# Performance work log

Measured on AMD Instinct MI355X. Metric: run time of the kernel, lower is better.

The kernel has to match this reference:

```python
import jax, jax.numpy as jnp
import numpy as np

EPS = 1e-08

def _householder(x, v):
    # x: [B,S,r], v: [B,S,r]; H x = x - 2 v_n (v_n . x), v_n = v/||v||
    v_norm_sq = jnp.sum(v * v, axis=-1, keepdims=True) + EPS
    v_n = v / jnp.sqrt(v_norm_sq)
    vTx = jnp.sum(x * v_n, axis=-1, keepdims=True)
    return x - 2.0 * v_n * vTx

def setup_inputs() -> dict:
    key = jax.random.key(0)
    ks = jax.random.split(key, 8)
    B, S, D, R = 4, 4096, 1024, 256
    N_IN, N_PROC, N_OUT, K = 16, 64, 16, 8
    x = jax.random.normal(ks[0], (B, S, D), dtype=jnp.float32)
    input_idx = jax.random.randint(ks[1], (B, S), 0, N_IN)
    process_indices = jax.random.randint(ks[2], (B, S, K), 0, N_PROC)
    output_idx = jax.random.randint(ks[3], (B, S), 0, N_OUT)
    # learned params (orthogonal-ish init approximated by scaled gaussian)
    input_neurons = jax.random.normal(ks[4], (N_IN, D, R), dtype=jnp.float32) / np.sqrt(D)
    pv = jax.random.normal(ks[5], (N_PROC, R), dtype=jnp.float32)
    process_neurons = pv / (jnp.linalg.norm(pv, axis=-1, keepdims=True) + EPS)
    output_neurons = jax.random.normal(ks[6], (N_OUT, R, D), dtype=jnp.float32) / np.sqrt(D)
    return {"x": x, "input_neurons": input_neurons, "process_neurons": process_neurons,
            "output_neurons": output_neurons, "input_idx": input_idx,
            "process_indices": process_indices, "output_idx": output_idx}

def reference(x, input_neurons, process_neurons, output_neurons,
              input_idx, process_indices, output_idx):
    # ---- input projection (hard selection): d_model -> rank ----
    # compute all-expert projections then gather per token (avoids [B,S,D,R] gather)
    all_in = jnp.einsum('bsd,ndr->bsnr', x, input_neurons)          # [B,S,n_in,R]
    h = jnp.take_along_axis(all_in, input_idx[..., None, None], axis=2)[:, :, 0, :]  # [B,S,R]
    # ---- process: k sequential Householder reflections ----
    selected_v = process_neurons[process_indices]                    # [B,S,k,R]
    vs = jnp.moveaxis(selected_v, 2, 0)                              # [k,B,S,R]
    def step(carry, v):
        return _householder(carry, v), None
    h, _ = jax.lax.scan(step, h, vs)
    # ---- output projection (hard selection): rank -> d_model ----
    all_out = jnp.einsum('bsr,nrd->bsnd', h, output_neurons)         # [B,S,n_out,D]
    out = jnp.take_along_axis(all_out, output_idx[..., None, None], axis=2)[:, :, 0, :]
    return out
```

## Files before the change

### kernel.cpp

```cpp
#include <hip/hip_runtime.h>
#include <hip/hip_bf16.h>

#define NT    16384
#define DM    1024
#define RK    256
#define N_IN  16
#define N_OUT 16
#define KHH   8
#define MAXTOK 1536
#define BM    64
#define TPE   (MAXTOK / BM)
#define KC    4

typedef short bf16x8 __attribute__((ext_vector_type(8)));
typedef float f32x4 __attribute__((ext_vector_type(4)));
typedef unsigned short u16;
typedef u16 u16x8 __attribute__((ext_vector_type(8)));
typedef u16 u16x4 __attribute__((ext_vector_type(4)));

__device__ __forceinline__ u16 f2bf(float f) {
  __hip_bfloat16 b = __float2bfloat16(f);
  return *reinterpret_cast<u16*>(&b);
}
__device__ __forceinline__ float bf2f(u16 u) {
  return __uint_as_float((unsigned)u << 16);
}

__device__ __forceinline__ void gl_lds16(const void* g, void* lds) {
  __builtin_amdgcn_global_load_lds(
      (const __attribute__((address_space(1))) void*)g,
      (__attribute__((address_space(3))) void*)lds, 16, 0, 0);
}

__global__ __launch_bounds__(256) void build_lists_pn(
    const int* __restrict__ in_idx, const int* __restrict__ out_idx,
    const float* __restrict__ pn,
    int* __restrict__ list_in, int* __restrict__ cnt_in,
    int* __restrict__ list_out, int* __restrict__ cnt_out,
    float* __restrict__ pnorm2) {
  const int b = blockIdx.x;
  const int tid = threadIdx.x, lane = tid & 63, wid = tid >> 6;

  if (b == 32) {
    const int p = tid >> 2, q = tid & 3;
    const float* row = pn + (size_t)p * RK + q * 64;
    float s = 0.f;
#pragma unroll
    for (int i = 0; i < 16; i++) {
      const float4 v = ((const float4*)row)[i];
      s += v.x * v.x + v.y * v.y + v.z * v.z + v.w * v.w;
    }
    s += __shfl_xor(s, 1);
    s += __shfl_xor(s, 2);
    if (q == 0) pnorm2[p] = s + 1e-8f;
    return;
  }

  const int e = b & 15, which = b >> 4;
  const int* __restrict__ idx = which ? out_idx : in_idx;
  int* __restrict__ list = (which ? list_out : list_in) + (size_t)e * NT;
  int* __restrict__ cnt = (which ? cnt_out : cnt_in) + e;

  __shared__ int wsum[4];
  const unsigned long long lt = (1ull << lane) - 1ull;
  int off = 0;
  for (int base = 0; base < NT; base += 1024) {
    const int4 iv = ((const int4*)(idx + base))[tid];
    const bool f0 = iv.x == e, f1 = iv.y == e, f2 = iv.z == e, f3 = iv.w == e;
    const unsigned long long m0 = __ballot(f0), m1 = __ballot(f1),
                             m2 = __ballot(f2), m3 = __ballot(f3);
    const int below = __popcll(m0 & lt) + __popcll(m1 & lt) +
                      __popcll(m2 & lt) + __popcll(m3 & lt);
    const int wtot = __popcll(m0) + __popcll(m1) + __popcll(m2) + __popcll(m3);
    if (lane == 0) wsum[wid] = wtot;
    __syncthreads();
    int b0 = 0, tot = 0;
#pragma unroll
    for (int w = 0; w < 4; w++) { if (w < wid) b0 += wsum[w]; tot += wsum[w]; }
    int pos = off + b0 + below;
    const int t = base + tid * 4;
    if (f0) list[pos++] = t;
    if (f1) list[pos++] = t + 1;
    if (f2) list[pos++] = t + 2;
    if (f3) list[pos++] = t + 3;
    off += tot;
    __syncthreads();
  }
  if (tid == 0) *cnt = off;
}

__global__ __launch_bounds__(256) void transpose_cvt2(
    const float* __restrict__ Win, const float* __restrict__ Wout,
    u16* __restrict__ WinT, u16* __restrict__ WoT) {
  const int z = blockIdx.z;
  const float* __restrict__ src = z ? Wout : Win;
  u16* __restrict__ dst = z ? WoT : WinT;
  const int R = z ? RK : DM, C = z ? DM : RK;
  const int e = blockIdx.y;
  const int tilesC = C >> 6;
  const int tr = (blockIdx.x / tilesC) << 6;
  const int tc = (blockIdx.x % tilesC) << 6;
  __shared__ float ls[64][65];
  const int t = threadIdx.x;
  const int row = t >> 2, q = t & 3;
  const float* s = src + (size_t)e * R * C + (size_t)(tr + row) * C + tc + q * 16;
#pragma unroll
  for (int j = 0; j < 4; j++) {
    const float4 v = ((const float4*)s)[j];
    ls[row][q * 16 + j * 4 + 0] = v.x;
    ls[row][q * 16 + j * 4 + 1] = v.y;
    ls[row][q * 16 + j * 4 + 2] = v.z;
    ls[row][q * 16 + j * 4 + 3] = v.w;
  }
  __syncthreads();
  const int cc = t >> 2;
  u16x8 o0, o1;
#pragma unroll
  for (int j = 0; j < 8; j++) o0[j] = f2bf(ls[q * 16 + j][cc]);
#pragma unroll
  for (int j = 0; j < 8; j++) o1[j] = f2bf(ls[q * 16 + 8 + j][cc]);
  u16* d = dst + (size_t)e * C * R + (size_t)(tc + cc) * R + tr + q * 16;
  ((u16x8*)d)[0] = o0;
  ((u16x8*)d)[1] = o1;
}

__global__ __launch_bounds__(256, 6) void input_gemm_part(
    const float* __restrict__ x, const u16* __restrict__ WinT,
    const int* __restrict__ list, const int* __restrict__ cnt,
    u16* __restrict__ h4) {
  const int bid = blockIdx.x;
  const int xcd = bid & 7;
  int j = bid >> 3;
  const int tile = j % TPE;
  j /= TPE;
  const int nb = j & 1;
  const int e = xcd * 2 + ((j >> 1) & 1);
  const int kc = j >> 2;
  const int nt = cnt[e];
  const int t0 = tile * BM;
  if (t0 >= nt) return;
  const int* __restrict__ lst = list + (size_t)e * NT + t0;
  const int ntok = min(BM, nt - t0);

  __shared__ __align__(16) u16 As[BM * 64];
  __shared__ __align__(16) u16 Bs[128 * 64];
  __shared__ int toks[BM];

  const int tid = threadIdx.x, lane = tid & 63, w = tid >> 6;
  if (tid < BM) toks[tid] = lst[tid < ntok ? tid : 0];
  __syncthreads();

  const int arow = tid >> 3, k8 = tid & 7;
  const float* axp0 = x + (size_t)toks[arow] * DM + kc * 256 + k8 * 8;
  const float* axp1 = x + (size_t)toks[arow + 32] * DM + kc * 256 + k8 * 8;
  const int aoff0 = arow * 128 + ((k8 ^ (arow & 7)) << 4);
  const int aoff1 = (arow + 32) * 128 + ((k8 ^ (arow & 7)) << 4);

  const int sub = lane >> 3;
  const int swz8 = ((lane & 7) ^ sub) * 8;
  const u16* Wbase = WinT + (size_t)e * RK * DM + (size_t)(nb * 128) * DM + kc * 256;

  f32x4 acc[4][2];
#pragma unroll
  for (int m = 0; m < 4; m++)
#pragma unroll
    for (int jx = 0; jx < 2; jx++) acc[m][jx] = (f32x4)0.f;

  const int l15 = lane & 15, lg = lane >> 4;

#pragma unroll
  for (int it = 0; it < 4; ++it) {
    const int k0 = it * 64;
    if (it) __syncthreads();
    const float4 p0a = ((const float4*)(axp0 + k0))[0];
    const float4 p0b = ((const float4*)(axp0 + k0))[1];
    const float4 p1a = ((const float4*)(axp1 + k0))[0];
    const float4 p1b = ((const float4*)(axp1 + k0))[1];
#pragma unroll
    for (int i = 0; i < 4; ++i) {
      const int g = w * 4 + i;
      const int n = g * 8 + sub;
      gl_lds16(Wbase + (size_t)n * DM + k0 + swz8, Bs + g * 512);
    }
    u16x8 av;
    av[0] = f2bf(p0a.x); av[1] = f2bf(p0a.y); av[2] = f2bf(p0a.z); av[3] = f2bf(p0a.w);
    av[4] = f2bf(p0b.x); av[5] = f2bf(p0b.y); av[6] = f2bf(p0b.z); av[7] = f2bf(p0b.w);
    *(u16x8*)((char*)As + aoff0) = av;
    av[0] = f2bf(p1a.x); av[1] = f2bf(p1a.y); av[2] = f2bf(p1a.z); av[3] = f2bf(p1a.w);
    av[4] = f2bf(p1b.x); av[5] = f2bf(p1b.y); av[6] = f2bf(p1b.z); av[7] = f2bf(p1b.w);
    *(u16x8*)((char*)As + aoff1) = av;
    __syncthreads();
#pragma unroll
    for (int kk = 0; kk < 2; ++kk) {
      const int sw = (((kk * 4 + lg) ^ (l15 & 7)) << 4);
      bf16x8 fa[4];
#pragma unroll
      for (int m = 0; m < 4; ++m)
        fa[m] = *(const bf16x8*)((const char*)As + (m * 16 + l15) * 128 + sw);
#pragma unroll
      for (int jx = 0; jx < 2; ++jx) {
        const int n = w * 32 + jx * 16 + l15;
        const bf16x8 fb = *(const bf16x8*)((const char*)Bs + n * 128 + sw);
#pragma unroll
        for (int m = 0; m < 4; ++m)
          acc[m][jx] = __builtin_amdgcn_mfma_f32_16x16x32_bf16(fa[m], fb, acc[m][jx], 0, 0, 0);
      }
    }
  }

  u16* hp4 = h4 + (size_t)kc * NT * RK;
#pragma unroll
  for (int m = 0; m < 4; ++m)
#pragma unroll
    for (int r = 0; r < 4; ++r) {
      const int slot = m * 16 + lg * 4 + r;
      if (slot < ntok) {
        u16* hp = hp4 + (size_t)toks[slot] * RK + nb * 128 + w * 32 + l15;
#pragma unroll
        for (int jx = 0; jx < 2; ++jx) hp[jx * 16] = f2bf(acc[m][jx][r]);
      }
    }
}

__global__ __launch_bounds__(256) void hh_k(
    const u16* __restrict__ h4, u16* __restrict__ hb,
    const float* __restrict__ pn, const float* __restrict__ pnorm2,
    const int* __restrict__ pidx) {
  const int lane = threadIdx.x & 63;
  const int t = blockIdx.x * 4 + (threadIdx.x >> 6);

  float4 hv;
  {
    const u16x4 p0 = ((const u16x4*)(h4 + ((size_t)0 * NT + t) * RK))[lane];
    const u16x4 p1 = ((const u16x4*)(h4 + ((size_t)1 * NT + t) * RK))[lane];
    const u16x4 p2 = ((const u16x4*)(h4 + ((size_t)2 * NT + t) * RK))[lane];
    const u16x4 p3 = ((const u16x4*)(h4 + ((size_t)3 * NT + t) * RK))[lane];
    hv.x = (bf2f(p0[0]) + bf2f(p1[0])) + (bf2f(p2[0]) + bf2f(p3[0]));
    hv.y = (bf2f(p0[1]) + bf2f(p1[1])) + (bf2f(p2[1]) + bf2f(p3[1]));
    hv.z = (bf2f(p0[2]) + bf2f(p1[2])) + (bf2f(p2[2]) + bf2f(p3[2]));
    hv.w = (bf2f(p0[3]) + bf2f(p1[3])) + (bf2f(p2[3]) + bf2f(p3[3]));
  }

#pragma unroll
  for (int k = 0; k < KHH; k++) {
    const int p = pidx[t * KHH + k];
    const float4 v = ((const float4*)(pn + (size_t)p * RK))[lane];
    float dvh = v.x * hv.x + v.y * hv.y + v.z * hv.z + v.w * hv.w;
#pragma unroll
    for (int s = 32; s; s >>= 1) dvh += __shfl_xor(dvh, s);
    const float c = 2.f * dvh / pnorm2[p];
    hv.x = fmaf(-c, v.x, hv.x);
    hv.y = fmaf(-c, v.y, hv.y);
    hv.z = fmaf(-c, v.z, hv.z);
    hv.w = fmaf(-c, v.w, hv.w);
  }
  u16x4 o;
  o[0] = f2bf(hv.x); o[1] = f2bf(hv.y); o[2] = f2bf(hv.z); o[3] = f2bf(hv.w);
  ((u16x4*)(hb + (size_t)t * RK))[lane] = o;
}

__global__ __launch_bounds__(256, 6) void output_gemm_mfma(
    const u16* __restrict__ hb, const u16* __restrict__ WoT,
    const int* __restrict__ list, const int* __restrict__ cnt,
    float* __restrict__ out) {
  const int bid = blockIdx.x;
  const int xcd = bid & 7;
  int j = bid >> 3;
  const int tile = j % TPE;
  j /= TPE;
  const int e = xcd * 2 + (j & 1);
  const int cb = j >> 1;
  const int nt = cnt[e];
  const int t0 = tile * BM;
  if (t0 >= nt) return;
  const int* __restrict__ lst = list + (size_t)e * NT + t0;
  const int ntok = min(BM, nt - t0);

  __shared__ __align__(16) u16 As[BM * 64];
  __shared__ __align__(16) u16 Bs[128 * 64];
  __shared__ int toks[BM];

  const int tid = threadIdx.x, lane = tid & 63, w = tid >> 6;
  if (tid < BM) toks[tid] = lst[tid < ntok ? tid : 0];
  __syncthreads();

  const int sub = lane >> 3;
  const int swz8 = ((lane & 7) ^ sub) * 8;
  const u16* Wbase = WoT + (size_t)e * DM * RK + (size_t)(cb * 128) * RK;
  const int ar0 = (w * 2 + 0) * 8 + sub;
  const int ar1 = (w * 2 + 1) * 8 + sub;
  const u16* asrc0 = hb + (size_t)toks[ar0] * RK + swz8;
  const u16* asrc1 = hb + (size_t)toks[ar1] * RK + swz8;

  f32x4 acc[4][2];
#pragma unroll
  for (int m = 0; m < 4; m++)
#pragma unroll
    for (int jx = 0; jx < 2; jx++) acc[m][jx] = (f32x4)0.f;

  const int l15 = lane & 15, lg = lane >> 4;

#pragma unroll
  for (int it = 0; it < RK / 64; ++it) {
    const int k0 = it * 64;
    if (it) __syncthreads();
    gl_lds16(asrc0 + k0, As + (w * 2 + 0) * 512);
    gl_lds16(asrc1 + k0, As + (w * 2 + 1) * 512);
#pragma unroll
    for (int i = 0; i < 4; ++i) {
      const int g = w * 4 + i;
      const int n = g * 8 + sub;
      gl_lds16(Wbase + (size_t)n * RK + k0 + swz8, Bs + g * 512);
    }
    __syncthreads();
#pragma unroll
    for (int kk = 0; kk < 2; ++kk) {
      const int sw = (((kk * 4 + lg) ^ (l15 & 7)) << 4);
      bf16x8 fa[4];
#pragma unroll
      for (int m = 0; m < 4; ++m)
        fa[m] = *(const bf16x8*)((const char*)As + (m * 16 + l15) * 128 + sw);
#pragma unroll
      for (int jx = 0; jx < 2; ++jx) {
        const int n = w * 32 + jx * 16 + l15;
        const bf16x8 fb = *(const bf16x8*)((const char*)Bs + n * 128 + sw);
#pragma unroll
        for (int m = 0; m < 4; ++m)
          acc[m][jx] = __builtin_amdgcn_mfma_f32_16x16x32_bf16(fa[m], fb, acc[m][jx], 0, 0, 0);
      }
    }
  }

#pragma unroll
  for (int m = 0; m < 4; ++m)
#pragma unroll
    for (int r = 0; r < 4; ++r) {
      const int slot = m * 16 + lg * 4 + r;
      if (slot < ntok) {
        float* op = out + (size_t)toks[slot] * DM + cb * 128 + w * 32 + l15;
#pragma unroll
        for (int jx = 0; jx < 2; ++jx) op[jx * 16] = acc[m][jx][r];
      }
    }
}

extern "C" void kernel_launch(void* const* d_in, const int* in_sizes, int n_in,
                              void* d_out, int out_size, void* d_ws,
                              size_t ws_size, hipStream_t stream) {
  const float* x     = (const float*)d_in[0];
  const float* Win   = (const float*)d_in[1];
  const float* pn    = (const float*)d_in[2];
  const float* Wout  = (const float*)d_in[3];
  const int* in_idx  = (const int*)d_in[4];
  const int* pidx    = (const int*)d_in[5];
  const int* out_idx = (const int*)d_in[6];
  float* out = (float*)d_out;

  char* ws = (char*)d_ws;
  u16* WinT  = (u16*)ws;                    ws += (size_t)N_IN * RK * DM * 2;
  u16* WoT   = (u16*)ws;                    ws += (size_t)N_OUT * DM * RK * 2;
  u16* hb    = (u16*)ws;                    ws += (size_t)NT * RK * 2;
  u16* h4    = (u16*)ws;                    ws += (size_t)KC * NT * RK * 2;
  int* list_in  = (int*)ws;                 ws += (size_t)N_IN * NT * 4;
  int* list_out = (int*)ws;                 ws += (size_t)N_OUT * NT * 4;
  int* cnt_in   = (int*)ws;                 ws += 64;
  int* cnt_out  = (int*)ws;                 ws += 64;
  float* pnorm2 = (float*)ws;

  hipLaunchKernelGGL(build_lists_pn, dim3(33), dim3(256), 0, stream,
                     in_idx, out_idx, pn, list_in, cnt_in, list_out, cnt_out,
                     pnorm2);
  hipLaunchKernelGGL(transpose_cvt2, dim3(64, 16, 2), dim3(256), 0, stream,
                     Win, Wout, WinT, WoT);
  hipLaunchKernelGGL(input_gemm_part, dim3(8 * TPE * 16), dim3(256), 0,
                     stream, x, WinT, list_in, cnt_in, h4);
  hipLaunchKernelGGL(hh_k, dim3(NT / 4), dim3(256), 0, stream,
                     h4, hb, pn, pnorm2, pidx);
  hipLaunchKernelGGL(output_gemm_mfma, dim3(8 * TPE * 16), dim3(256), 0,
                     stream, hb, WoT, list_out, cnt_out, out);
}
```

Measured before the change: 84.93 us.

## Preload full A tile and double-buffer B loads in expert GEMMs

Both routed GEMM kernels now stage the entire 64x256 A tile into LDS once, up front. The weight (B) tiles are double-buffered with async global-to-LDS loads, and waits use s_waitcnt vmcnt instead of per-iteration __syncthreads. This is safe because each wave loads exactly the B rows it later reads. The aim is to overlap weight fetches with MFMA work and remove the block barriers inside the K loop. In exchange, LDS per block grows to about 64KB and the occupancy hint drops from 6 to 2 blocks per CU, leaving less latency hiding from concurrent blocks.

```diff
diff --git a/kernel.cpp b/kernel.cpp
--- a/kernel.cpp
+++ b/kernel.cpp
@@ -124,7 +124,7 @@
   ((u16x8*)d)[1] = o1;
 }
 
-__global__ __launch_bounds__(256, 6) void input_gemm_part(
+__global__ __launch_bounds__(256, 2) void input_gemm_part(
     const float* __restrict__ x, const u16* __restrict__ WinT,
     const int* __restrict__ list, const int* __restrict__ cnt,
     u16* __restrict__ h4) {
@@ -142,24 +142,48 @@
   const int* __restrict__ lst = list + (size_t)e * NT + t0;
   const int ntok = min(BM, nt - t0);
 
-  __shared__ __align__(16) u16 As[BM * 64];
-  __shared__ __align__(16) u16 Bs[128 * 64];
+  __shared__ __align__(16) u16 As[64 * 256];
+  __shared__ __align__(16) u16 Bs[2 * 128 * 64];
   __shared__ int toks[BM];
 
   const int tid = threadIdx.x, lane = tid & 63, w = tid >> 6;
   if (tid < BM) toks[tid] = lst[tid < ntok ? tid : 0];
   __syncthreads();
 
-  const int arow = tid >> 3, k8 = tid & 7;
-  const float* axp0 = x + (size_t)toks[arow] * DM + kc * 256 + k8 * 8;
-  const float* axp1 = x + (size_t)toks[arow + 32] * DM + kc * 256 + k8 * 8;
-  const int aoff0 = arow * 128 + ((k8 ^ (arow & 7)) << 4);
-  const int aoff1 = (arow + 32) * 128 + ((k8 ^ (arow & 7)) << 4);
-
   const int sub = lane >> 3;
   const int swz8 = ((lane & 7) ^ sub) * 8;
   const u16* Wbase = WinT + (size_t)e * RK * DM + (size_t)(nb * 128) * DM + kc * 256;
 
+#define BSTAGE(it_, buf_)                                                 \
+  do {                                                                    \
+    _Pragma("unroll") for (int i_ = 0; i_ < 4; ++i_) {                    \
+      const int g_ = w * 4 + i_;                                          \
+      const int n_ = g_ * 8 + sub;                                        \
+      gl_lds16(Wbase + (size_t)n_ * DM + (it_) * 64 + swz8,               \
+               Bs + (buf_) * 8192 + g_ * 512);                            \
+    }                                                                     \
+  } while (0)
+
+  BSTAGE(0, 0);
+
+  {
+    const int row = tid >> 2, q = tid & 3;
+    const float* xp = x + (size_t)toks[row] * DM + kc * 256 + q * 64;
+    float4 xv[16];
+#pragma unroll
+    for (int i = 0; i < 16; ++i) xv[i] = ((const float4*)xp)[i];
+#pragma unroll
+    for (int s7 = 0; s7 < 8; ++s7) {
+      const float4 a = xv[s7 * 2], b2 = xv[s7 * 2 + 1];
+      u16x8 o;
+      o[0] = f2bf(a.x); o[1] = f2bf(a.y); o[2] = f2bf(a.z); o[3] = f2bf(a.w);
+      o[4] = f2bf(b2.x); o[5] = f2bf(b2.y); o[6] = f2bf(b2.z); o[7] = f2bf(b2.w);
+      const int phys = q * 8 + (s7 ^ (row & 7));
+      *(u16x8*)((char*)As + row * 512 + phys * 16) = o;
+    }
+  }
+  __syncthreads();
+
   f32x4 acc[4][2];
 #pragma unroll
   for (int m = 0; m < 4; m++)
@@ -170,43 +194,32 @@
 
 #pragma unroll
   for (int it = 0; it < 4; ++it) {
-    const int k0 = it * 64;
-    if (it) __syncthreads();
-    const float4 p0a = ((const float4*)(axp0 + k0))[0];
-    const float4 p0b = ((const float4*)(axp0 + k0))[1];
-    const float4 p1a = ((const float4*)(axp1 + k0))[0];
-    const float4 p1b = ((const float4*)(axp1 + k0))[1];
-#pragma unroll
-    for (int i = 0; i < 4; ++i) {
-      const int g = w * 4 + i;
-      const int n = g * 8 + sub;
-      gl_lds16(Wbase + (size_t)n * DM + k0 + swz8, Bs + g * 512);
-    }
-    u16x8 av;
-    av[0] = f2bf(p0a.x); av[1] = f2bf(p0a.y); av[2] = f2bf(p0a.z); av[3] = f2bf(p0a.w);
-    av[4] = f2bf(p0b.x); av[5] = f2bf(p0b.y); av[6] = f2bf(p0b.z); av[7] = f2bf(p0b.w);
-    *(u16x8*)((char*)As + aoff0) = av;
-    av[0] = f2bf(p1a.x); av[1] = f2bf(p1a.y); av[2] = f2bf(p1a.z); av[3] = f2bf(p1a.w);
-    av[4] = f2bf(p1b.x); av[5] = f2bf(p1b.y); av[6] = f2bf(p1b.z); av[7] = f2bf(p1b.w);
-    *(u16x8*)((char*)As + aoff1) = av;
-    __syncthreads();
+    if (it < 3) BSTAGE(it + 1, (it + 1) & 1);
+    if (it < 3)
+      asm volatile("s_waitcnt vmcnt(4)" ::: "memory");
+    else
+      asm volatile("s_waitcnt vmcnt(0)" ::: "memory");
+    __builtin_amdgcn_sched_barrier(0);
+    const char* Bb = (const char*)Bs + (it & 1) * 16384;
 #pragma unroll
     for (int kk = 0; kk < 2; ++kk) {
+      const int phys = it * 8 + ((kk * 4 + lg) ^ (l15 & 7));
+      bf16x8 fa[4];
+#pragma unroll
+      for (int m = 0; m < 4; ++m)
+        fa[m] = *(const bf16x8*)((const char*)As + (m * 16 + l15) * 512 + phys * 16);
       const int sw = (((kk * 4 + lg) ^ (l15 & 7)) << 4);
-      bf16x8 fa[4];
-#pragma unroll
-      for (int m = 0; m < 4; ++m)
-        fa[m] = *(const bf16x8*)((const char*)As + (m * 16 + l15) * 128 + sw);
 #pragma unroll
       for (int jx = 0; jx < 2; ++jx) {
         const int n = w * 32 + jx * 16 + l15;
-        const bf16x8 fb = *(const bf16x8*)((const char*)Bs + n * 128 + sw);
+        const bf16x8 fb = *(const bf16x8*)(Bb + n * 128 + sw);
 #pragma unroll
         for (int m = 0; m < 4; ++m)
           acc[m][jx] = __builtin_amdgcn_mfma_f32_16x16x32_bf16(fa[m], fb, acc[m][jx], 0, 0, 0);
       }
     }
   }
+#undef BSTAGE
 
   u16* hp4 = h4 + (size_t)kc * NT * RK;
 #pragma unroll
@@ -259,7 +272,7 @@
   ((u16x4*)(hb + (size_t)t * RK))[lane] = o;
 }
 
-__global__ __launch_bounds__(256, 6) void output_gemm_mfma(
+__global__ __launch_bounds__(256, 2) void output_gemm_mfma(
     const u16* __restrict__ hb, const u16* __restrict__ WoT,
     const int* __restrict__ list, const int* __restrict__ cnt,
     float* __restrict__ out) {
@@ -276,8 +289,8 @@
   const int* __restrict__ lst = list + (size_t)e * NT + t0;
   const int ntok = min(BM, nt - t0);
 
-  __shared__ __align__(16) u16 As[BM * 64];
-  __shared__ __align__(16) u16 Bs[128 * 64];
+  __shared__ __align__(16) u16 As[64 * 256];
+  __shared__ __align__(16) u16 Bs[2 * 128 * 64];
   __shared__ int toks[BM];
 
   const int tid = threadIdx.x, lane = tid & 63, w = tid >> 6;
@@ -287,10 +300,27 @@
   const int sub = lane >> 3;
   const int swz8 = ((lane & 7) ^ sub) * 8;
   const u16* Wbase = WoT + (size_t)e * DM * RK + (size_t)(cb * 128) * RK;
-  const int ar0 = (w * 2 + 0) * 8 + sub;
-  const int ar1 = (w * 2 + 1) * 8 + sub;
-  const u16* asrc0 = hb + (size_t)toks[ar0] * RK + swz8;
-  const u16* asrc1 = hb + (size_t)toks[ar1] * RK + swz8;
+
+#define BSTAGE(it_, buf_)                                                 \
+  do {                                                                    \
+    _Pragma("unroll") for (int i_ = 0; i_ < 4; ++i_) {                    \
+      const int g_ = w * 4 + i_;                                          \
+      const int n_ = g_ * 8 + sub;                                        \
+      gl_lds16(Wbase + (size_t)n_ * RK + (it_) * 64 + swz8,               \
+               Bs + (buf_) * 8192 + g_ * 512);                            \
+    }                                                                     \
+  } while (0)
+
+  BSTAGE(0, 0);
+#pragma unroll
+  for (int i = 0; i < 8; ++i) {
+    const int v = w * 8 + i;
+    const int row = v * 2 + (lane >> 5);
+    const int slot = lane & 31;
+    const int sl = (slot & 24) | ((slot & 7) ^ (row & 7));
+    gl_lds16(hb + (size_t)toks[row] * RK + sl * 8, As + v * 512);
+  }
+  __syncthreads();
 
   f32x4 acc[4][2];
 #pragma unroll
@@ -301,35 +331,33 @@
   const int l15 = lane & 15, lg = lane >> 4;
 
 #pragma unroll
-  for (int it = 0; it < RK / 64; ++it) {
-    const int k0 = it * 64;
-    if (it) __syncthreads();
-    gl_lds16(asrc0 + k0, As + (w * 2 + 0) * 512);
-    gl_lds16(asrc1 + k0, As + (w * 2 + 1) * 512);
-#pragma unroll
-    for (int i = 0; i < 4; ++i) {
-      const int g = w * 4 + i;
-      const int n = g * 8 + sub;
-      gl_lds16(Wbase + (size_t)n * RK + k0 + swz8, Bs + g * 512);
-    }
-    __syncthreads();
+  for (int it = 0; it < 4; ++it) {
+    if (it < 3) BSTAGE(it + 1, (it + 1) & 1);
+    if (it < 3)
+      asm volatile("s_waitcnt vmcnt(4)" ::: "memory");
+    else
+      asm volatile("s_waitcnt vmcnt(0)" ::: "memory");
+    __builtin_amdgcn_sched_barrier(0);
+    const char* Bb = (const char*)Bs + (it & 1) * 16384;
 #pragma unroll
     for (int kk = 0; kk < 2; ++kk) {
+      const int phys = it * 8 + ((kk * 4 + lg) ^ (l15 & 7));
+      bf16x8 fa[4];
+#pragma unroll
+      for (int m = 0; m < 4; ++m)
+        fa[m] = *(const bf16x8*)((const char*)As + (m * 16 + l15) * 512 + phys * 16);
       const int sw = (((kk * 4 + lg) ^ (l15 & 7)) << 4);
-      bf16x8 fa[4];
-#pragma unroll
-      for (int m = 0; m < 4; ++m)
-        fa[m] = *(const bf16x8*)((const char*)As + (m * 16 + l15) * 128 + sw);
 #pragma unroll
       for (int jx = 0; jx < 2; ++jx) {
         const int n = w * 32 + jx * 16 + l15;
-        const bf16x8 fb = *(const bf16x8*)((const char*)Bs + n * 128 + sw);
+        const bf16x8 fb = *(const bf16x8*)(Bb + n * 128 + sw);
 #pragma unroll
         for (int m = 0; m < 4; ++m)
           acc[m][jx] = __builtin_amdgcn_mfma_f32_16x16x32_bf16(fa[m], fb, acc[m][jx], 0, 0, 0);
       }
     }
   }
+#undef BSTAGE
 
 #pragma unroll
   for (int m = 0; m < 4; ++m)
```

Measured after the change: 102.1 us. 20.2% more time.
